# Optimization experiments

Hardware: AMD Instinct MI355X
Metric: run time of the kernel (lower is better)

Reference implementation:

```python
import jax, jax.numpy as jnp
import numpy as np

N = 50000
E = 800000
IN_DIM, HID_DIM, OUT_DIM = 128, 64, 32


def _gcn_layer(x, src, dst, norm, W, b, n):
    # GCNConv: h = D^{-1/2}(A+I)D^{-1/2} (x W) + b
    h = x @ W  # [n, d_out]
    agg = jax.ops.segment_sum(h[src] * norm[:, None], dst, num_segments=n)
    return agg + b


def _backbone(x, edge_index, W1, b1, W2, b2):
    n = x.shape[0]
    loop = jnp.arange(n)
    src = jnp.concatenate([edge_index[0], loop])  # add self-loops
    dst = jnp.concatenate([edge_index[1], loop])
    deg = jax.ops.segment_sum(jnp.ones(src.shape[0], x.dtype), dst, num_segments=n)
    dinv = jax.lax.rsqrt(deg)  # deg >= 1 thanks to self-loops
    norm = dinv[src] * dinv[dst]  # symmetric normalization per edge
    h = jax.nn.relu(_gcn_layer(x, src, dst, norm, W1, b1, n))
    return _gcn_layer(h, src, dst, norm, W2, b2, n)


def _zscore_cols(h):
    # torch: (h - h.mean(0)) / h.std(0), std is unbiased (ddof=1)
    mean = h.mean(0)
    std = jnp.sqrt(jnp.sum((h - mean) ** 2, axis=0) / (h.shape[0] - 1))
    return (h - mean) / std


def setup_inputs() -> dict:
    key = jax.random.key(0)
    k1, k2, k3, k4, k5, k6 = jax.random.split(key, 6)
    x1 = jax.random.normal(k1, (N, IN_DIM), dtype=jnp.float32)
    x2 = jax.random.normal(k2, (N, IN_DIM), dtype=jnp.float32)
    edge_index1 = jax.random.randint(k3, (2, E), 0, N, dtype=jnp.int64 if jax.config.jax_enable_x64 else jnp.int32)
    edge_index2 = jax.random.randint(k4, (2, E), 0, N, dtype=jnp.int64 if jax.config.jax_enable_x64 else jnp.int32)
    W1 = jax.random.normal(k5, (IN_DIM, HID_DIM), dtype=jnp.float32) * (1.0 / np.sqrt(IN_DIM))
    W2 = jax.random.normal(k6, (HID_DIM, OUT_DIM), dtype=jnp.float32) * (1.0 / np.sqrt(HID_DIM))
    b1 = jnp.zeros((HID_DIM,), jnp.float32)
    b2 = jnp.zeros((OUT_DIM,), jnp.float32)
    return {"x1": x1, "edge_index1": edge_index1, "x2": x2, "edge_index2": edge_index2,
            "W1": W1, "b1": b1, "W2": W2, "b2": b2}


def reference(x1, edge_index1, x2, edge_index2, W1, b1, W2, b2):
    h1 = _backbone(x1, edge_index1, W1, b1, W2, b2)
    h2 = _backbone(x2, edge_index2, W1, b1, W2, b2)
    z1 = _zscore_cols(h1)
    z2 = _zscore_cols(h2)
    return (z1, z2)
```

## Files before the change

kernel.cpp:

```cpp
#include <hip/hip_runtime.h>
#include <hip/hip_fp16.h>
#include <math.h>

#define IN_DIM 128
#define HID 64
#define OUTD 32
#define BSH 8
#define BSZ 256
#define EPB 4096
#define XPAD 136
#define NCOPY 16

typedef __attribute__((ext_vector_type(8))) _Float16 f16x8;
typedef __attribute__((ext_vector_type(4))) float f32x4;

struct GB {
    const int* src; const int* dst;
    int* bh;
    int* btot;
    unsigned int* pairs;
    int* rowptr; int* csr_src;
    float* dinv;
    double* st;
    float* og;
    _Float16* o16;
    const float* x;
    _Float16* hs;
    __half* h2;
};

__global__ void __launch_bounds__(256) k_hist(GB g0, GB g1, const float* __restrict__ W,
                                              _Float16* __restrict__ wt16, int e, int nb, int nbh) {
    int tid = threadIdx.x;
    int bx = blockIdx.x;
    if (bx == 2 * nbh) {
        for (int i = tid; i < HID * IN_DIM; i += 256) {
            int d = i >> 7, k = i & 127;
            wt16[i] = (_Float16)W[k * HID + d];
        }
        return;
    }
    const GB& g = (bx >= nbh) ? g1 : g0;
    int blk = (bx >= nbh) ? bx - nbh : bx;
    __shared__ int hist[512];
    for (int i = tid; i < nb; i += 256) hist[i] = 0;
    __syncthreads();
    int base = blk * EPB;
#pragma unroll
    for (int k = 0; k < EPB / 256; ++k) {
        int idx = base + k * 256 + tid;
        if (idx < e) atomicAdd(&hist[g.dst[idx] >> BSH], 1);
    }
    __syncthreads();
    int* row = g.bh + (size_t)blk * nb;
    for (int i = tid; i < nb; i += 256) row[i] = hist[i];
}

__global__ void k_colscan(GB g0, GB g1, int nb, int nbh) {
    const GB& g = blockIdx.y ? g1 : g0;
    __shared__ int ls[256];
    int tid = threadIdx.x;
    int b = blockIdx.x;
    int v = (tid < nbh) ? g.bh[(size_t)tid * nb + b] : 0;
    ls[tid] = v;
    __syncthreads();
    for (int off = 1; off < 256; off <<= 1) {
        int u = (tid >= off) ? ls[tid - off] : 0;
        __syncthreads();
        ls[tid] += u;
        __syncthreads();
    }
    if (tid < nbh) g.bh[(size_t)tid * nb + b] = ls[tid] - v;
    if (tid == 255) g.btot[b] = ls[255];
    if (b < 4) {
        int i = b * 256 + tid;
        g.st[i] = 0.0;
    }
}

__global__ void __launch_bounds__(256) k_p2mm(GB g0, GB g1, const _Float16* __restrict__ wt16,
                                              int e, int n, int nb, int nbh, int slotsP, int nmm) {
    __shared__ char smem[2 * 64 * XPAD * 2];
    int tid = threadIdx.x;
    int bx = blockIdx.x;
    if (bx < slotsP) {
        const GB& g = ((bx & 7) >= 4) ? g1 : g0;
        int blk = (bx >> 3) * 4 + (bx & 3);
        if (blk >= nbh) return;
        int* sc = (int*)smem;
        int* lcur = (int*)(smem + 1024);
        int v = (tid < nb) ? g.btot[tid] : 0;
        sc[tid] = v;
        __syncthreads();
        for (int off = 1; off < 256; off <<= 1) {
            int u = (tid >= off) ? sc[tid - off] : 0;
            __syncthreads();
            sc[tid] += u;
            __syncthreads();
        }
        int excl = sc[tid] - v;
        __syncthreads();
        sc[tid] = excl;
        __syncthreads();
        const int* row = g.bh + (size_t)blk * nb;
        for (int i = tid; i < nb; i += 256) lcur[i] = sc[i] + row[i];
        __syncthreads();
        int base = blk * EPB;
#pragma unroll
        for (int k = 0; k < EPB / 256; ++k) {
            int idx = base + k * 256 + tid;
            if (idx < e) {
                int s = g.src[idx], d = g.dst[idx];
                int pos = atomicAdd(&lcur[d >> BSH], 1);
                g.pairs[pos] = (unsigned int)s | ((unsigned int)(d & (BSZ - 1)) << 24);
            }
        }
    } else {
        int mx = bx - slotsP;
        const GB& g = (mx >= nmm) ? g1 : g0;
        int blk = (mx >= nmm) ? mx - nmm : mx;
        _Float16 (*xs)[XPAD] = (_Float16(*)[XPAD])smem;
        _Float16 (*wt)[XPAD] = (_Float16(*)[XPAD])(smem + 64 * XPAD * 2);
        int node0 = blk * 64;
        {
            const f16x8* Wg = (const f16x8*)wt16;
#pragma unroll
            for (int j = 0; j < 4; ++j) {
                int i = tid + 256 * j;
                int d = i >> 4, koff = (i & 15) * 8;
                *(f16x8*)&wt[d][koff] = Wg[i];
            }
        }
        {
            const float4* X4 = (const float4*)g.x;
#pragma unroll
            for (int j = 0; j < 8; ++j) {
                int i = tid + 256 * j;
                int row = i >> 5, c4 = i & 31;
                int gn = node0 + row;
                float4 v = (gn < n) ? X4[(size_t)gn * 32 + c4] : make_float4(0.f, 0.f, 0.f, 0.f);
                _Float16* p = &xs[row][c4 * 4];
                p[0] = (_Float16)v.x; p[1] = (_Float16)v.y;
                p[2] = (_Float16)v.z; p[3] = (_Float16)v.w;
            }
        }
        __syncthreads();
        int wv = tid >> 6, lane = tid & 63;
        int r16 = lane & 15, khi = lane >> 4;
        int wnode0 = wv * 16;
        f32x4 acc[4] = {};
#pragma unroll
        for (int kk = 0; kk < 4; ++kk) {
            f16x8 a = *(const f16x8*)&xs[wnode0 + r16][kk * 32 + khi * 8];
#pragma unroll
            for (int nt = 0; nt < 4; ++nt) {
                f16x8 b = *(const f16x8*)&wt[nt * 16 + r16][kk * 32 + khi * 8];
                acc[nt] = __builtin_amdgcn_mfma_f32_16x16x32_f16(a, b, acc[nt], 0, 0, 0);
            }
        }
#pragma unroll
        for (int r = 0; r < 4; ++r) {
            int node = node0 + wnode0 + khi * 4 + r;
            if (node < n) {
#pragma unroll
                for (int nt = 0; nt < 4; ++nt)
                    g.hs[(size_t)node * HID + nt * 16 + r16] = (_Float16)acc[nt][r];
            }
        }
    }
}

__global__ void __launch_bounds__(256) k_local_csr(GB g0, GB g1, int n, int e, int nb) {
    int bx = blockIdx.x;
    const GB& g = ((bx & 7) >= 4) ? g1 : g0;
    int b = (bx >> 3) * 4 + (bx & 3);
    if (b >= nb) return;
    __shared__ int sc[256], ldeg[BSZ], lrow[BSZ];
    __shared__ float ldv[BSZ];
    int tid = threadIdx.x;
    int v = (tid < nb) ? g.btot[tid] : 0;
    sc[tid] = v;
    __syncthreads();
    for (int off = 1; off < 256; off <<= 1) {
        int u = (tid >= off) ? sc[tid - off] : 0;
        __syncthreads();
        sc[tid] += u;
        __syncthreads();
    }
    int excl = sc[tid] - v;
    __syncthreads();
    sc[tid] = excl;
    __syncthreads();
    int node0 = b << BSH;
    int lo = sc[b], hi = lo + g.btot[b];
    ldeg[tid] = 0;
    __syncthreads();
    for (int j = lo + tid; j < hi; j += 256)
        atomicAdd(&ldeg[g.pairs[j] >> 24], 1);
    __syncthreads();
    int d = ldeg[tid];
    lrow[tid] = d;
    __syncthreads();
    for (int off = 1; off < BSZ; off <<= 1) {
        int u = (tid >= off) ? lrow[tid - off] : 0;
        __syncthreads();
        lrow[tid] += u;
        __syncthreads();
    }
    int node = node0 + tid;
    if (node < n) {
        g.rowptr[node] = lo + lrow[tid] - d;
        float dvv = rsqrtf((float)(d + 1));
        g.dinv[node] = dvv;
        ldv[tid] = dvv;
    } else {
        ldv[tid] = 0.0f;
    }
    lrow[tid] = lo + lrow[tid] - d;
    __syncthreads();
    for (int j = lo + tid; j < hi; j += 256) {
        unsigned int w = g.pairs[j];
        int pos = atomicAdd(&lrow[w >> 24], 1);
        g.csr_src[pos] = (int)(w & 0xFFFFFFu);
    }
    if (b == 0 && tid == 0) g.rowptr[n] = e;
    __half2* Hv = (__half2*)g.hs;
    for (int i = tid; i < BSZ * (HID / 2); i += 256) {
        int row = i >> 5;
        int nd = node0 + row;
        if (nd < n) {
            float scv = ldv[row];
            size_t idx = (size_t)nd * (HID / 2) + (i & 31);
            float2 vv = __half22float2(Hv[idx]);
            Hv[idx] = __floats2half2_rn(vv.x * scv, vv.y * scv);
        }
    }
}

__global__ void __launch_bounds__(256) k_gather_fuse(GB g0, GB g1, const float* __restrict__ b1,
                                                     const float* __restrict__ W2, int n, int nblkg) {
    int bx = blockIdx.x;
    const GB& g = ((bx & 7) >= 4) ? g1 : g0;
    int blk = (bx >> 3) * 4 + (bx & 3);
    if (blk >= nblkg) return;
    __shared__ float sh[32][HID + 1];
    __shared__ float w2s[HID][OUTD];
    __shared__ float bs[HID];
    int tid = threadIdx.x;
    for (int i = tid; i < HID * OUTD; i += 256) w2s[i >> 5][i & 31] = W2[i];
    if (tid < HID) bs[tid] = b1[tid];
    int l8 = tid & 7, gi = tid >> 3;
    int node = blk * 32 + gi;
    float a[8] = {};
    if (node < n) {
        const f16x8* H = (const f16x8*)g.hs;
        f16x8 v = H[(size_t)node * 8 + l8];
#pragma unroll
        for (int k = 0; k < 8; ++k) a[k] = (float)v[k];
        int lo = g.rowptr[node], hi = g.rowptr[node + 1];
        int j = lo;
        for (; j + 8 <= hi; j += 8) {
            int s0 = g.csr_src[j],     s1 = g.csr_src[j + 1];
            int s2 = g.csr_src[j + 2], s3 = g.csr_src[j + 3];
            int s4 = g.csr_src[j + 4], s5 = g.csr_src[j + 5];
            int s6 = g.csr_src[j + 6], s7 = g.csr_src[j + 7];
            f16x8 v0 = H[(size_t)s0 * 8 + l8];
            f16x8 v1 = H[(size_t)s1 * 8 + l8];
            f16x8 v2 = H[(size_t)s2 * 8 + l8];
            f16x8 v3 = H[(size_t)s3 * 8 + l8];
            f16x8 v4 = H[(size_t)s4 * 8 + l8];
            f16x8 v5 = H[(size_t)s5 * 8 + l8];
            f16x8 v6 = H[(size_t)s6 * 8 + l8];
            f16x8 v7 = H[(size_t)s7 * 8 + l8];
            f16x8 s01 = v0 + v1, s23 = v2 + v3, s45 = v4 + v5, s67 = v6 + v7;
            f16x8 s = (s01 + s23) + (s45 + s67);
#pragma unroll
            for (int k = 0; k < 8; ++k) a[k] += (float)s[k];
        }
        if (j + 4 <= hi) {
            int s0 = g.csr_src[j],     s1 = g.csr_src[j + 1];
            int s2 = g.csr_src[j + 2], s3 = g.csr_src[j + 3];
            f16x8 v0 = H[(size_t)s0 * 8 + l8];
            f16x8 v1 = H[(size_t)s1 * 8 + l8];
            f16x8 v2 = H[(size_t)s2 * 8 + l8];
            f16x8 v3 = H[(size_t)s3 * 8 + l8];
            f16x8 s = (v0 + v1) + (v2 + v3);
#pragma unroll
            for (int k = 0; k < 8; ++k) a[k] += (float)s[k];
            j += 4;
        }
        for (; j < hi; ++j) {
            f16x8 v0 = H[(size_t)g.csr_src[j] * 8 + l8];
#pragma unroll
            for (int k = 0; k < 8; ++k) a[k] += (float)v0[k];
        }
    }
    __syncthreads();
    if (node < n) {
        float dv = g.dinv[node];
#pragma unroll
        for (int k = 0; k < 8; ++k)
            a[k] = fmaxf(fmaf(a[k], dv, bs[l8 * 8 + k]), 0.0f);
    }
#pragma unroll
    for (int k = 0; k < 8; ++k) sh[gi][l8 * 8 + k] = a[k];
    __syncthreads();
    int n2 = tid >> 3, fo = (tid & 7) * 4;
    int node2 = blk * 32 + n2;
    if (node2 < n) {
        float a0 = 0.f, a1 = 0.f, a2 = 0.f, a3 = 0.f;
#pragma unroll
        for (int k = 0; k < HID; ++k) {
            float s = sh[n2][k];
            a0 = fmaf(s, w2s[k][fo], a0);
            a1 = fmaf(s, w2s[k][fo + 1], a1);
            a2 = fmaf(s, w2s[k][fo + 2], a2);
            a3 = fmaf(s, w2s[k][fo + 3], a3);
        }
        float dv2 = g.dinv[node2];
        __half2* H2 = (__half2*)g.h2;
        H2[(size_t)node2 * (OUTD / 2) + (fo >> 1)]     = __floats2half2_rn(a0 * dv2, a1 * dv2);
        H2[(size_t)node2 * (OUTD / 2) + (fo >> 1) + 1] = __floats2half2_rn(a2 * dv2, a3 * dv2);
    }
}

__global__ void __launch_bounds__(256) k_gather2s(GB g0, GB g1, int n, int nblkg) {
    int bx = blockIdx.x;
    const GB& g = ((bx & 7) >= 4) ? g1 : g0;
    int blk = (bx >> 3) * 4 + (bx & 3);
    if (blk >= nblkg) return;
    __shared__ float sx[64][33], sq[64][33];
    int tid = threadIdx.x;
    int l4 = tid & 3, gi = tid >> 2;
    int node = blk * 64 + gi;
    float a[8] = {};
    if (node < n) {
        const f16x8* H = (const f16x8*)g.h2;
        f16x8 v = H[(size_t)node * 4 + l4];
#pragma unroll
        for (int k = 0; k < 8; ++k) a[k] = (float)v[k];
        int lo = g.rowptr[node], hi = g.rowptr[node + 1];
        int j = lo;
        for (; j + 8 <= hi; j += 8) {
            int s0 = g.csr_src[j],     s1 = g.csr_src[j + 1];
            int s2 = g.csr_src[j + 2], s3 = g.csr_src[j + 3];
            int s4 = g.csr_src[j + 4], s5 = g.csr_src[j + 5];
            int s6 = g.csr_src[j + 6], s7 = g.csr_src[j + 7];
            f16x8 v0 = H[(size_t)s0 * 4 + l4];
            f16x8 v1 = H[(size_t)s1 * 4 + l4];
            f16x8 v2 = H[(size_t)s2 * 4 + l4];
            f16x8 v3 = H[(size_t)s3 * 4 + l4];
            f16x8 v4 = H[(size_t)s4 * 4 + l4];
            f16x8 v5 = H[(size_t)s5 * 4 + l4];
            f16x8 v6 = H[(size_t)s6 * 4 + l4];
            f16x8 v7 = H[(size_t)s7 * 4 + l4];
            f16x8 s01 = v0 + v1, s23 = v2 + v3, s45 = v4 + v5, s67 = v6 + v7;
            f16x8 s = (s01 + s23) + (s45 + s67);
#pragma unroll
            for (int k = 0; k < 8; ++k) a[k] += (float)s[k];
        }
        if (j + 4 <= hi) {
            int s0 = g.csr_src[j],     s1 = g.csr_src[j + 1];
            int s2 = g.csr_src[j + 2], s3 = g.csr_src[j + 3];
            f16x8 v0 = H[(size_t)s0 * 4 + l4];
            f16x8 v1 = H[(size_t)s1 * 4 + l4];
            f16x8 v2 = H[(size_t)s2 * 4 + l4];
            f16x8 v3 = H[(size_t)s3 * 4 + l4];
            f16x8 s = (v0 + v1) + (v2 + v3);
#pragma unroll
            for (int k = 0; k < 8; ++k) a[k] += (float)s[k];
            j += 4;
        }
        for (; j < hi; ++j) {
            f16x8 v0 = H[(size_t)g.csr_src[j] * 4 + l4];
#pragma unroll
            for (int k = 0; k < 8; ++k) a[k] += (float)v0[k];
        }
        float dv = g.dinv[node];
#pragma unroll
        for (int k = 0; k < 8; ++k) a[k] *= dv;
        f16x8 o;
#pragma unroll
        for (int k = 0; k < 8; ++k) o[k] = (_Float16)a[k];
        ((f16x8*)g.o16)[(size_t)node * 4 + l4] = o;
    }
#pragma unroll
    for (int k = 0; k < 8; ++k) {
        sx[gi][l4 * 8 + k] = a[k];
        sq[gi][l4 * 8 + k] = a[k] * a[k];
    }
    __syncthreads();
    if (tid < 64) {
        int c = tid & 31;
        bool isq = tid >= 32;
        float s = 0.0f;
        for (int r = 0; r < 64; ++r) s += isq ? sq[r][c] : sx[r][c];
        atomicAdd(&g.st[(blk & (NCOPY - 1)) * 64 + c + (isq ? 32 : 0)], (double)s);
    }
}

__global__ void k_transform(GB g0, GB g1, int n) {
    const GB& g = blockIdx.y ? g1 : g0;
    __shared__ float fm[32], fr[32];
    int tid = threadIdx.x;
    if (tid < 32) {
        double sum = 0.0, sqs = 0.0;
#pragma unroll
        for (int k = 0; k < NCOPY; ++k) {
            sum += g.st[k * 64 + tid];
            sqs += g.st[k * 64 + tid + 32];
        }
        double mean = sum / (double)n;
        double var = (sqs - sum * sum / (double)n) / (double)(n - 1);
        fm[tid] = (float)mean;
        fr[tid] = (float)(1.0 / sqrt(var));
    }
    __syncthreads();
    int t4 = (blockIdx.x * 256 + tid) * 4;
    if (t4 < n * OUTD) {
        const __half2* O = (const __half2*)g.o16;
        float2 u0 = __half22float2(O[t4 / 2]);
        float2 u1 = __half22float2(O[t4 / 2 + 1]);
        int c = t4 & 31;
        float4 r;
        r.x = (u0.x - fm[c])     * fr[c];
        r.y = (u0.y - fm[c + 1]) * fr[c + 1];
        r.z = (u1.x - fm[c + 2]) * fr[c + 2];
        r.w = (u1.y - fm[c + 3]) * fr[c + 3];
        *(float4*)&g.og[t4] = r;
    }
}


extern "C" void kernel_launch(void* const* d_in, const int* in_sizes, int n_in,
                              void* d_out, int out_size, void* d_ws, size_t ws_size,
                              hipStream_t stream) {
    const float* x1 = (const float*)d_in[0];
    const int*   ei1 = (const int*)d_in[1];
    const float* x2 = (const float*)d_in[2];
    const int*   ei2 = (const int*)d_in[3];
    const float* W1 = (const float*)d_in[4];
    const float* b1 = (const float*)d_in[5];
    const float* W2 = (const float*)d_in[6];
    const float* b2 = (const float*)d_in[7];
    (void)b2;
    (void)n_in; (void)out_size; (void)ws_size;

    int n = in_sizes[0] / IN_DIM;
    int e = in_sizes[1] / 2;
    float* out = (float*)d_out;
    int nb  = (n + BSZ - 1) >> BSH;
    int nbh = (e + EPB - 1) / EPB;
    int nmm = (n + 63) / 64;

    char* ws = (char*)d_ws;
    size_t off = 0;
    auto alloc = [&](size_t bytes) {
        void* p = ws + off;
        off = (off + bytes + 255) & ~(size_t)255;
        return p;
    };
    int*    bh_base   = (int*)alloc((size_t)2 * nbh * nb * 4);
    int*    btot_base = (int*)alloc((size_t)2 * nb * 4);
    double* st_base   = (double*)alloc((size_t)2 * NCOPY * 64 * 8);
    _Float16* o16_base = (_Float16*)alloc((size_t)2 * n * OUTD * 2);
    _Float16* wt16     = (_Float16*)alloc((size_t)HID * IN_DIM * 2);

    GB G[2];
    for (int g = 0; g < 2; ++g) {
        const int* ei = g ? ei2 : ei1;
        G[g].src  = ei;
        G[g].dst  = ei + e;
        G[g].x    = g ? x2 : x1;
        G[g].bh   = bh_base + (size_t)g * nbh * nb;
        G[g].btot = btot_base + (size_t)g * nb;
        G[g].st   = st_base + (size_t)g * NCOPY * 64;
        G[g].o16  = o16_base + (size_t)g * n * OUTD;
        G[g].rowptr  = (int*)alloc(((size_t)n + 1) * 4);
        G[g].csr_src = (int*)alloc((size_t)e * 4);
        G[g].dinv    = (float*)alloc((size_t)n * 4);
        G[g].og      = out + (size_t)g * n * OUTD;
        G[g].hs      = (_Float16*)alloc((size_t)n * HID * 2);
    }
    size_t pairs_bytes = (size_t)2 * e * 4;
    size_t h2_bytes    = (size_t)2 * n * OUTD * 2;
    char* uni = (char*)alloc(pairs_bytes > h2_bytes ? pairs_bytes : h2_bytes);
    G[0].pairs = (unsigned int*)uni;
    G[1].pairs = G[0].pairs + e;
    G[0].h2 = (__half*)uni;
    G[1].h2 = G[0].h2 + (size_t)n * OUTD;

    k_hist<<<dim3(2 * nbh + 1), 256, 0, stream>>>(G[0], G[1], W1, wt16, e, nb, nbh);
    k_colscan<<<dim3(nb, 2), 256, 0, stream>>>(G[0], G[1], nb, nbh);
    int slotsP = ((nbh + 3) / 4) * 8;
    k_p2mm<<<dim3(slotsP + 2 * nmm), 256, 0, stream>>>(G[0], G[1], wt16, e, n, nb, nbh, slotsP, nmm);
    int slotsC = ((nb + 3) / 4) * 8;
    k_local_csr<<<dim3(slotsC), BSZ, 0, stream>>>(G[0], G[1], n, e, nb);

    int nblkg1 = (n + 31) / 32;
    int slots1 = ((nblkg1 + 3) / 4) * 8;
    k_gather_fuse<<<dim3(slots1), 256, 0, stream>>>(G[0], G[1], b1, W2, n, nblkg1);
    int nblkg2 = (n + 63) / 64;
    int slots2 = ((nblkg2 + 3) / 4) * 8;
    k_gather2s<<<dim3(slots2), 256, 0, stream>>>(G[0], G[1], n, nblkg2);

    k_transform<<<dim3((n * OUTD / 4 + 255) / 256, 2), 256, 0, stream>>>(G[0], G[1], n);
}
```

Baseline: 119.1 us.

## Split layer-1 features into two 32-wide halves and gather each pass separately

The layer-1 hidden features are now stored as two separate N×32 fp16 arrays instead of one N×64 array. The first gather kernel handles 64 nodes per block with 4 lanes per node and walks the neighbour list twice, once per half. Each pass touches a smaller working set (about 3.2 MB per half per graph), which is meant to improve L2/cache hit rates for the random neighbour gathers. In exchange the CSR indices are read twice, and the second matmul now computes 8 outputs per thread.

```diff
diff --git a/kernel.cpp b/kernel.cpp
--- a/kernel.cpp
+++ b/kernel.cpp
@@ -25,7 +25,8 @@
     float* og;
     _Float16* o16;
     const float* x;
-    _Float16* hs;
+    _Float16* hsA;
+    _Float16* hsB;
     __half* h2;
 };
 
@@ -163,8 +164,10 @@
             int node = node0 + wnode0 + khi * 4 + r;
             if (node < n) {
 #pragma unroll
-                for (int nt = 0; nt < 4; ++nt)
-                    g.hs[(size_t)node * HID + nt * 16 + r16] = (_Float16)acc[nt][r];
+                for (int nt = 0; nt < 4; ++nt) {
+                    _Float16* dst = (nt < 2) ? g.hsA : g.hsB;
+                    dst[(size_t)node * 32 + (nt & 1) * 16 + r16] = (_Float16)acc[nt][r];
+                }
             }
         }
     }
@@ -224,15 +227,18 @@
         g.csr_src[pos] = (int)(w & 0xFFFFFFu);
     }
     if (b == 0 && tid == 0) g.rowptr[n] = e;
-    __half2* Hv = (__half2*)g.hs;
-    for (int i = tid; i < BSZ * (HID / 2); i += 256) {
-        int row = i >> 5;
+    __half2* HA = (__half2*)g.hsA;
+    __half2* HB = (__half2*)g.hsB;
+    for (int i = tid; i < BSZ * 16; i += 256) {
+        int row = i >> 4;
         int nd = node0 + row;
         if (nd < n) {
             float scv = ldv[row];
-            size_t idx = (size_t)nd * (HID / 2) + (i & 31);
-            float2 vv = __half22float2(Hv[idx]);
-            Hv[idx] = __floats2half2_rn(vv.x * scv, vv.y * scv);
+            size_t idx = (size_t)nd * 16 + (i & 15);
+            float2 va = __half22float2(HA[idx]);
+            HA[idx] = __floats2half2_rn(va.x * scv, va.y * scv);
+            float2 vb = __half22float2(HB[idx]);
+            HB[idx] = __floats2half2_rn(vb.x * scv, vb.y * scv);
         }
     }
 }
@@ -243,84 +249,85 @@
     const GB& g = ((bx & 7) >= 4) ? g1 : g0;
     int blk = (bx >> 3) * 4 + (bx & 3);
     if (blk >= nblkg) return;
-    __shared__ float sh[32][HID + 1];
+    __shared__ float sh[64][HID + 1];
     __shared__ float w2s[HID][OUTD];
     __shared__ float bs[HID];
     int tid = threadIdx.x;
     for (int i = tid; i < HID * OUTD; i += 256) w2s[i >> 5][i & 31] = W2[i];
     if (tid < HID) bs[tid] = b1[tid];
-    int l8 = tid & 7, gi = tid >> 3;
-    int node = blk * 32 + gi;
-    float a[8] = {};
-    if (node < n) {
-        const f16x8* H = (const f16x8*)g.hs;
-        f16x8 v = H[(size_t)node * 8 + l8];
-#pragma unroll
-        for (int k = 0; k < 8; ++k) a[k] = (float)v[k];
-        int lo = g.rowptr[node], hi = g.rowptr[node + 1];
-        int j = lo;
-        for (; j + 8 <= hi; j += 8) {
-            int s0 = g.csr_src[j],     s1 = g.csr_src[j + 1];
-            int s2 = g.csr_src[j + 2], s3 = g.csr_src[j + 3];
-            int s4 = g.csr_src[j + 4], s5 = g.csr_src[j + 5];
-            int s6 = g.csr_src[j + 6], s7 = g.csr_src[j + 7];
-            f16x8 v0 = H[(size_t)s0 * 8 + l8];
-            f16x8 v1 = H[(size_t)s1 * 8 + l8];
-            f16x8 v2 = H[(size_t)s2 * 8 + l8];
-            f16x8 v3 = H[(size_t)s3 * 8 + l8];
-            f16x8 v4 = H[(size_t)s4 * 8 + l8];
-            f16x8 v5 = H[(size_t)s5 * 8 + l8];
-            f16x8 v6 = H[(size_t)s6 * 8 + l8];
-            f16x8 v7 = H[(size_t)s7 * 8 + l8];
-            f16x8 s01 = v0 + v1, s23 = v2 + v3, s45 = v4 + v5, s67 = v6 + v7;
-            f16x8 s = (s01 + s23) + (s45 + s67);
-#pragma unroll
-            for (int k = 0; k < 8; ++k) a[k] += (float)s[k];
-        }
-        if (j + 4 <= hi) {
-            int s0 = g.csr_src[j],     s1 = g.csr_src[j + 1];
-            int s2 = g.csr_src[j + 2], s3 = g.csr_src[j + 3];
-            f16x8 v0 = H[(size_t)s0 * 8 + l8];
-            f16x8 v1 = H[(size_t)s1 * 8 + l8];
-            f16x8 v2 = H[(size_t)s2 * 8 + l8];
-            f16x8 v3 = H[(size_t)s3 * 8 + l8];
-            f16x8 s = (v0 + v1) + (v2 + v3);
-#pragma unroll
-            for (int k = 0; k < 8; ++k) a[k] += (float)s[k];
-            j += 4;
-        }
-        for (; j < hi; ++j) {
-            f16x8 v0 = H[(size_t)g.csr_src[j] * 8 + l8];
-#pragma unroll
-            for (int k = 0; k < 8; ++k) a[k] += (float)v0[k];
-        }
-    }
-    __syncthreads();
-    if (node < n) {
-        float dv = g.dinv[node];
-#pragma unroll
-        for (int k = 0; k < 8; ++k)
-            a[k] = fmaxf(fmaf(a[k], dv, bs[l8 * 8 + k]), 0.0f);
-    }
-#pragma unroll
-    for (int k = 0; k < 8; ++k) sh[gi][l8 * 8 + k] = a[k];
-    __syncthreads();
-    int n2 = tid >> 3, fo = (tid & 7) * 4;
-    int node2 = blk * 32 + n2;
+    int l4 = tid & 3, gi = tid >> 2;
+    int node = blk * 64 + gi;
+    int lo = 0, hi = 0; float dv = 0.0f;
+    if (node < n) { lo = g.rowptr[node]; hi = g.rowptr[node + 1]; dv = g.dinv[node]; }
+    __syncthreads();
+#pragma unroll
+    for (int p = 0; p < 2; ++p) {
+        const f16x8* H = (const f16x8*)(p ? g.hsB : g.hsA);
+        float a[8] = {};
+        if (node < n) {
+            f16x8 v = H[(size_t)node * 4 + l4];
+#pragma unroll
+            for (int k = 0; k < 8; ++k) a[k] = (float)v[k];
+            int j = lo;
+            for (; j + 8 <= hi; j += 8) {
+                int s0 = g.csr_src[j],     s1 = g.csr_src[j + 1];
+                int s2 = g.csr_src[j + 2], s3 = g.csr_src[j + 3];
+                int s4 = g.csr_src[j + 4], s5 = g.csr_src[j + 5];
+                int s6 = g.csr_src[j + 6], s7 = g.csr_src[j + 7];
+                f16x8 v0 = H[(size_t)s0 * 4 + l4];
+                f16x8 v1 = H[(size_t)s1 * 4 + l4];
+                f16x8 v2 = H[(size_t)s2 * 4 + l4];
+                f16x8 v3 = H[(size_t)s3 * 4 + l4];
+                f16x8 v4 = H[(size_t)s4 * 4 + l4];
+                f16x8 v5 = H[(size_t)s5 * 4 + l4];
+                f16x8 v6 = H[(size_t)s6 * 4 + l4];
+                f16x8 v7 = H[(size_t)s7 * 4 + l4];
+                f16x8 s01 = v0 + v1, s23 = v2 + v3, s45 = v4 + v5, s67 = v6 + v7;
+                f16x8 s = (s01 + s23) + (s45 + s67);
+#pragma unroll
+                for (int k = 0; k < 8; ++k) a[k] += (float)s[k];
+            }
+            if (j + 4 <= hi) {
+                int s0 = g.csr_src[j],     s1 = g.csr_src[j + 1];
+                int s2 = g.csr_src[j + 2], s3 = g.csr_src[j + 3];
+                f16x8 v0 = H[(size_t)s0 * 4 + l4];
+                f16x8 v1 = H[(size_t)s1 * 4 + l4];
+                f16x8 v2 = H[(size_t)s2 * 4 + l4];
+                f16x8 v3 = H[(size_t)s3 * 4 + l4];
+                f16x8 s = (v0 + v1) + (v2 + v3);
+#pragma unroll
+                for (int k = 0; k < 8; ++k) a[k] += (float)s[k];
+                j += 4;
+            }
+            for (; j < hi; ++j) {
+                f16x8 v0 = H[(size_t)g.csr_src[j] * 4 + l4];
+#pragma unroll
+                for (int k = 0; k < 8; ++k) a[k] += (float)v0[k];
+            }
+#pragma unroll
+            for (int k = 0; k < 8; ++k)
+                a[k] = fmaxf(fmaf(a[k], dv, bs[p * 32 + l4 * 8 + k]), 0.0f);
+        }
+#pragma unroll
+        for (int k = 0; k < 8; ++k) sh[gi][p * 32 + l4 * 8 + k] = a[k];
+    }
+    __syncthreads();
+    int n2 = tid >> 2, f8 = (tid & 3) * 8;
+    int node2 = blk * 64 + n2;
     if (node2 < n) {
-        float a0 = 0.f, a1 = 0.f, a2 = 0.f, a3 = 0.f;
+        float acc[8] = {};
 #pragma unroll
         for (int k = 0; k < HID; ++k) {
             float s = sh[n2][k];
-            a0 = fmaf(s, w2s[k][fo], a0);
-            a1 = fmaf(s, w2s[k][fo + 1], a1);
-            a2 = fmaf(s, w2s[k][fo + 2], a2);
-            a3 = fmaf(s, w2s[k][fo + 3], a3);
+#pragma unroll
+            for (int j = 0; j < 8; ++j) acc[j] = fmaf(s, w2s[k][f8 + j], acc[j]);
         }
         float dv2 = g.dinv[node2];
         __half2* H2 = (__half2*)g.h2;
-        H2[(size_t)node2 * (OUTD / 2) + (fo >> 1)]     = __floats2half2_rn(a0 * dv2, a1 * dv2);
-        H2[(size_t)node2 * (OUTD / 2) + (fo >> 1) + 1] = __floats2half2_rn(a2 * dv2, a3 * dv2);
+#pragma unroll
+        for (int j = 0; j < 4; ++j)
+            H2[(size_t)node2 * (OUTD / 2) + (f8 >> 1) + j] =
+                __floats2half2_rn(acc[2 * j] * dv2, acc[2 * j + 1] * dv2);
     }
 }
 
@@ -480,7 +487,8 @@
         G[g].csr_src = (int*)alloc((size_t)e * 4);
         G[g].dinv    = (float*)alloc((size_t)n * 4);
         G[g].og      = out + (size_t)g * n * OUTD;
-        G[g].hs      = (_Float16*)alloc((size_t)n * HID * 2);
+        G[g].hsA     = (_Float16*)alloc((size_t)n * 32 * 2);
+        G[g].hsB     = (_Float16*)alloc((size_t)n * 32 * 2);
     }
     size_t pairs_bytes = (size_t)2 * e * 4;
     size_t h2_bytes    = (size_t)2 * n * OUTD * 2;
@@ -497,7 +505,7 @@
     int slotsC = ((nb + 3) / 4) * 8;
     k_local_csr<<<dim3(slotsC), BSZ, 0, stream>>>(G[0], G[1], n, e, nb);
 
-    int nblkg1 = (n + 31) / 32;
+    int nblkg1 = (n + 63) / 64;
     int slots1 = ((nblkg1 + 3) / 4) * 8;
     k_gather_fuse<<<dim3(slots1), 256, 0, stream>>>(G[0], G[1], b1, W2, n, nblkg1);
     int nblkg2 = (n + 63) / 64;
```

Measured after the change: 127.2 us. 6.8% more time.
